# Performance work log

Measured on AMD Instinct MI355X. Metric: run time of the kernel, lower is better.

## Reference

```python
import jax, jax.numpy as jnp
import numpy as np

N_NODES = 100000
N_EDGES = 1600000
IN_FEA = 128
HIDDEN = 128
OUT_FEA = 40


def setup_inputs() -> dict:
    key = jax.random.key(0)
    k1, k2, k3, k4 = jax.random.split(key, 4)
    x = jax.random.normal(k1, (N_NODES, IN_FEA), dtype=jnp.float32)
    edge_index = jax.random.randint(k2, (2, N_EDGES), 0, N_NODES, dtype=jnp.int32)
    # Glorot-ish scaled weights
    W1 = jax.random.normal(k3, (IN_FEA, HIDDEN), dtype=jnp.float32) * (1.0 / np.sqrt(IN_FEA))
    b1 = jnp.zeros((HIDDEN,), dtype=jnp.float32)
    W2 = jax.random.normal(k4, (HIDDEN, OUT_FEA), dtype=jnp.float32) * (1.0 / np.sqrt(HIDDEN))
    b2 = jnp.zeros((OUT_FEA,), dtype=jnp.float32)
    return {"x": x, "edge_index": edge_index, "W1": W1, "b1": b1, "W2": W2, "b2": b2}


def _gcn_conv(x, src, dst, norm, W, b, n_nodes):
    # Linear transform first (PyG GCNConv order), then normalized scatter-add.
    h = x @ W                                   # [N, H]
    msg = h[src] * norm[:, None]                # [E+N, H] gather + scale
    out = jax.ops.segment_sum(msg, dst, num_segments=n_nodes)
    return out + b


def reference(x, edge_index, W1, b1, W2, b2):
    n = x.shape[0]
    loops = jnp.arange(n, dtype=edge_index.dtype)
    src = jnp.concatenate([edge_index[0], loops])  # add self-loops
    dst = jnp.concatenate([edge_index[1], loops])
    # Symmetric degree normalization: deg computed at destination (col)
    deg = jax.ops.segment_sum(jnp.ones_like(dst, dtype=x.dtype), dst, num_segments=n)
    dinv = jax.lax.rsqrt(jnp.maximum(deg, 1.0))
    norm = dinv[src] * dinv[dst]                # [E+N]

    h = jax.nn.relu(_gcn_conv(x, src, dst, norm, W1, b1, n))
    # dropout is identity in eval mode
    logits = _gcn_conv(h, src, dst, norm, W2, b2, n)
    return jax.nn.log_softmax(logits, axis=1)
```

## Files before the change

### kernel.cpp

```cpp
#include <hip/hip_runtime.h>
#include <math.h>

#define N_NODES 100000
#define N_EDGES 1600000
#define CHUNK 4096
#define NCH ((N_EDGES + CHUNK - 1) / CHUNK)
#define DSH 9
#define NBD ((N_NODES + 511) / 512)
#define CAP 9216
#define RCAP 10240

typedef __attribute__((ext_vector_type(8))) short bf16x8;
typedef __attribute__((ext_vector_type(4))) float f32x4;
typedef __attribute__((ext_vector_type(2))) float f32x2;

union U4S8 { uint4 u; bf16x8 s; };

__device__ inline unsigned pk_bf16(float a, float b) {
    unsigned ua = __float_as_uint(a), ub = __float_as_uint(b);
    ua = (ua + 0x7FFFu + ((ua >> 16) & 1u)) >> 16;
    ub = (ub + 0x7FFFu + ((ub >> 16) & 1u)) >> 16;
    return (ua & 0xFFFFu) | (ub << 16);
}
__device__ inline unsigned short bf16_1(float a) {
    unsigned ua = __float_as_uint(a);
    return (unsigned short)((ua + 0x7FFFu + ((ua >> 16) & 1u)) >> 16);
}

__device__ inline void acc8_fp8(f32x2* a, uint2 v) {
    a[0] += __builtin_amdgcn_cvt_pk_f32_fp8((int)v.x, false);
    a[1] += __builtin_amdgcn_cvt_pk_f32_fp8((int)v.x, true);
    a[2] += __builtin_amdgcn_cvt_pk_f32_fp8((int)v.y, false);
    a[3] += __builtin_amdgcn_cvt_pk_f32_fp8((int)v.y, true);
}

__device__ inline void gload_lds16(const void* g, void* l) {
    __builtin_amdgcn_global_load_lds(
        (const __attribute__((address_space(1))) unsigned*)g,
        (__attribute__((address_space(3))) unsigned*)l, 16, 0, 0);
}


__global__ __launch_bounds__(256) void k_prep(const float* __restrict__ W1, const float* __restrict__ W2,
                                              unsigned* __restrict__ W1t, unsigned* __restrict__ W2t,
                                              unsigned* __restrict__ Hb, unsigned* __restrict__ H2b) {
    __shared__ short L[16384];
    int t = threadIdx.x;
    if (blockIdx.x == 0) {
        for (int i = t; i < 16384; i += 256) {
            int k = i >> 7, n = i & 127;
            L[n * 128 + k] = (short)bf16_1(W1[i]);
        }
        __syncthreads();
        uint4* out = (uint4*)W1t;
        const uint4* src = (const uint4*)L;
        for (int i = t; i < 2048; i += 256) out[i] = src[i];
        if (t < 32) Hb[(size_t)N_NODES * 32 + t] = 0u;
    } else {
        for (int i = t; i < 48 * 128; i += 256) L[i] = 0;
        __syncthreads();
        for (int i = t; i < 5120; i += 256) {
            int k = i / 40, n = i - k * 40;
            L[n * 128 + k] = (short)bf16_1(W2[i]);
        }
        __syncthreads();
        uint4* out = (uint4*)W2t;
        const uint4* src = (const uint4*)L;
        for (int i = t; i < 768; i += 256) out[i] = src[i];
        if (t < 10) H2b[(size_t)N_NODES * 10 + t] = 0u;
    }
}


__global__ __launch_bounds__(256) void k_partD(const int* __restrict__ src, const int* __restrict__ dst,
                                               int* __restrict__ gtails, unsigned* __restrict__ staged, int E) {
    __shared__ int hist[NBD];
    __shared__ int tails[NBD];
    int t = threadIdx.x, c = blockIdx.x;
    if (t < NBD) hist[t] = 0;
    __syncthreads();
    int be = c * CHUNK, cw = min(CHUNK, E - be);
    int cw4 = cw >> 2;
    const int4* d4 = (const int4*)(dst + be);
    const int4* s4 = (const int4*)(src + be);
    for (int l = t; l < cw4; l += 256) {
        int4 d = d4[l];
        atomicAdd(&hist[d.x >> DSH], 1);
        atomicAdd(&hist[d.y >> DSH], 1);
        atomicAdd(&hist[d.z >> DSH], 1);
        atomicAdd(&hist[d.w >> DSH], 1);
    }
    __syncthreads();
    if (t < NBD) tails[t] = t * CAP + atomicAdd(&gtails[t], hist[t]);
    __syncthreads();
    for (int l = t; l < cw4; l += 256) {
        int4 d = d4[l];
        int4 s = s4[l];
        int i0 = atomicAdd(&tails[d.x >> DSH], 1);
        staged[i0] = ((unsigned)s.x << DSH) | (unsigned)(d.x & 511);
        int i1 = atomicAdd(&tails[d.y >> DSH], 1);
        staged[i1] = ((unsigned)s.y << DSH) | (unsigned)(d.y & 511);
        int i2 = atomicAdd(&tails[d.z >> DSH], 1);
        staged[i2] = ((unsigned)s.z << DSH) | (unsigned)(d.z & 511);
        int i3 = atomicAdd(&tails[d.w >> DSH], 1);
        staged[i3] = ((unsigned)s.w << DSH) | (unsigned)(d.w & 511);
    }
}

__global__ __launch_bounds__(256) void k_rank(const unsigned* __restrict__ staged, const int* __restrict__ gtails,
                                              int* __restrict__ csr, int* __restrict__ rowptr,
                                              int* __restrict__ cnt, float* __restrict__ dinv, int N) {
    __shared__ unsigned ebuf[RCAP];
    __shared__ int deg[512];
    __shared__ int sc[256];
    __shared__ int tails[512];
    int b = blockIdx.x, t = threadIdx.x;
    int n0 = b << DSH;
    int eb = b * CAP;
    int ne = gtails[b];
    deg[t] = 0; deg[t + 256] = 0;
    __syncthreads();
    bool fit = (ne <= RCAP);
    if (fit) {
        int ne4 = ne >> 2;
        const uint4* st4 = (const uint4*)(staged + eb);
        for (int l = t; l < ne4; l += 256) {
            uint4 pr = st4[l];
            ((uint4*)ebuf)[l] = pr;
            atomicAdd(&deg[pr.x & 511], 1);
            atomicAdd(&deg[pr.y & 511], 1);
            atomicAdd(&deg[pr.z & 511], 1);
            atomicAdd(&deg[pr.w & 511], 1);
        }
        for (int l = (ne4 << 2) + t; l < ne; l += 256) {
            unsigned pr = staged[eb + l];
            ebuf[l] = pr;
            atomicAdd(&deg[pr & 511], 1);
        }
    } else {
        for (int l = t; l < ne; l += 256)
            atomicAdd(&deg[staged[eb + l] & 511], 1);
    }
    __syncthreads();
    int d0 = deg[2 * t], d1 = deg[2 * t + 1];
    int ts = d0 + d1;
    sc[t] = ts; __syncthreads();
    for (int o = 1; o < 256; o <<= 1) {
        int v = (t >= o) ? sc[t - o] : 0;
        __syncthreads();
        sc[t] += v;
        __syncthreads();
    }
    int excl = sc[t] - ts;
    int na = n0 + 2 * t, nb = n0 + 2 * t + 1;
    tails[2 * t] = eb + excl;
    tails[2 * t + 1] = eb + excl + d0;
    if (na < N) { rowptr[na] = eb + excl;      cnt[na] = d0; dinv[na] = rsqrtf((float)(d0 + 1)); }
    if (nb < N) { rowptr[nb] = eb + excl + d0; cnt[nb] = d1; dinv[nb] = rsqrtf((float)(d1 + 1)); }
    __syncthreads();
    if (fit) {
        int ne4 = ne >> 2;
        for (int l = t; l < ne4; l += 256) {
            uint4 pr = ((const uint4*)ebuf)[l];
            int p0 = atomicAdd(&tails[pr.x & 511], 1); csr[p0] = (int)(pr.x >> DSH);
            int p1 = atomicAdd(&tails[pr.y & 511], 1); csr[p1] = (int)(pr.y >> DSH);
            int p2 = atomicAdd(&tails[pr.z & 511], 1); csr[p2] = (int)(pr.z >> DSH);
            int p3 = atomicAdd(&tails[pr.w & 511], 1); csr[p3] = (int)(pr.w >> DSH);
        }
        for (int l = (ne4 << 2) + t; l < ne; l += 256) {
            unsigned pr = ebuf[l];
            int pos = atomicAdd(&tails[pr & 511], 1);
            csr[pos] = (int)(pr >> DSH);
        }
    } else {
        for (int l = t; l < ne; l += 256) {
            unsigned pr = staged[eb + l];
            int pos = atomicAdd(&tails[pr & 511], 1);
            csr[pos] = (int)(pr >> DSH);
        }
    }
}


__global__ __launch_bounds__(256) void k_gemm1(const float* __restrict__ x, const unsigned* __restrict__ W1t,
                                               const float* __restrict__ dinv, unsigned* __restrict__ Hb, int M) {
    __shared__ uint4 As[2048];
    __shared__ uint4 Bs[2048];
    int t = threadIdx.x;
    int w = t >> 6, lane = t & 63;
    int m = lane & 15, kg = lane >> 4;
    int blk0 = blockIdx.x * 64;

    #pragma unroll
    for (int it = 0; it < 8; ++it) {
        int G = it * 256 + t;
        int row = G >> 5, slot = G & 31;
        int rowg = min(blk0 + row, M - 1);
        const float* srcp = x + (size_t)rowg * 128 + ((slot ^ (row & 7)) << 2);
        gload_lds16(srcp, (char*)As + (size_t)G * 16);
    }
    #pragma unroll
    for (int it = 0; it < 8; ++it) {
        int G = it * 256 + t;
        int rb = G >> 4, slot = G & 15;
        const unsigned* srcp = W1t + rb * 64 + ((slot ^ (rb & 7)) << 2);
        gload_lds16(srcp, (char*)Bs + (size_t)G * 16);
    }
    __syncthreads();

    int ra = (w << 4) + m;
    int rs = m & 7;
    f32x4 acc[8];
    #pragma unroll
    for (int j = 0; j < 8; j++) acc[j] = (f32x4){0.f, 0.f, 0.f, 0.f};

    #pragma unroll
    for (int ks = 0; ks < 4; ks++) {
        uint4 qa = As[ra * 32 + ((ks * 8 + kg * 2) ^ rs)];
        uint4 qb = As[ra * 32 + ((ks * 8 + kg * 2 + 1) ^ rs)];
        float4 f0 = *(float4*)&qa;
        float4 f1 = *(float4*)&qb;
        U4S8 a0; a0.u = make_uint4(pk_bf16(f0.x, f0.y), pk_bf16(f0.z, f0.w),
                                   pk_bf16(f1.x, f1.y), pk_bf16(f1.z, f1.w));
        #pragma unroll
        for (int nt = 0; nt < 8; nt++) {
            U4S8 b; b.u = Bs[(nt * 16 + m) * 16 + ((ks * 4 + kg) ^ rs)];
            acc[nt] = __builtin_amdgcn_mfma_f32_16x16x32_bf16(a0.s, b.s, acc[nt], 0, 0, 0);
        }
    }
    int m_base = blk0 + (w << 4);
    #pragma unroll
    for (int r = 0; r < 4; r++) {
        int row = m_base + kg * 4 + r;
        float di = dinv[min(row, M - 1)];
        bool on = (row < M) && ((m & 3) == 0);
        #pragma unroll
        for (int nt = 0; nt < 8; nt++) {
            float v = acc[nt][r] * di;
            float v1 = __shfl_xor(v, 1);
            unsigned wlo = (unsigned)__builtin_amdgcn_cvt_pk_fp8_f32(v, v1, 0, false);
            unsigned whi = __shfl_xor(wlo, 2);
            unsigned u = (wlo & 0xFFFFu) | (whi << 16);
            if (on) Hb[(size_t)row * 32 + nt * 4 + (m >> 2)] = u;
        }
    }
}


__global__ __launch_bounds__(256) void k_prop1(const unsigned* __restrict__ Hb, const int* __restrict__ rowptr,
                                               const int* __restrict__ cnt, const int* __restrict__ csr,
                                               const float* __restrict__ dinv, const float* __restrict__ b1,
                                               unsigned* __restrict__ h1b, int N) {
    int lane = threadIdx.x & 63;
    int g = lane >> 4, q = lane & 15;
    int i = blockIdx.x * 16 + (threadIdx.x >> 6) * 4 + g;
    if (i >= N) return;
    const uint2* H2 = (const uint2*)Hb;

    f32x2 a0[4], a1[4], a2[4], a3[4];
    #pragma unroll
    for (int k = 0; k < 4; k++) {
        a0[k] = (f32x2){0.f, 0.f}; a1[k] = (f32x2){0.f, 0.f};
        a2[k] = (f32x2){0.f, 0.f}; a3[k] = (f32x2){0.f, 0.f};
    }

    {
        uint2 sv = H2[(size_t)i * 16 + q];
        acc8_fp8(a0, sv);
    }

    int s = rowptr[i];
    int e = s + cnt[i];
    int p = s;
    for (; p + 8 <= e; p += 8) {
        int j0 = csr[p];     int j1 = csr[p + 1];
        int j2 = csr[p + 2]; int j3 = csr[p + 3];
        int j4 = csr[p + 4]; int j5 = csr[p + 5];
        int j6 = csr[p + 6]; int j7 = csr[p + 7];
        uint2 v0 = H2[(size_t)j0 * 16 + q];
        uint2 v1 = H2[(size_t)j1 * 16 + q];
        uint2 v2 = H2[(size_t)j2 * 16 + q];
        uint2 v3 = H2[(size_t)j3 * 16 + q];
        uint2 v4 = H2[(size_t)j4 * 16 + q];
        uint2 v5 = H2[(size_t)j5 * 16 + q];
        uint2 v6 = H2[(size_t)j6 * 16 + q];
        uint2 v7 = H2[(size_t)j7 * 16 + q];
        acc8_fp8(a0, v0); acc8_fp8(a1, v1); acc8_fp8(a2, v2); acc8_fp8(a3, v3);
        acc8_fp8(a0, v4); acc8_fp8(a1, v5); acc8_fp8(a2, v6); acc8_fp8(a3, v7);
    }
    if (p + 4 <= e) {
        int j0 = csr[p];     int j1 = csr[p + 1];
        int j2 = csr[p + 2]; int j3 = csr[p + 3];
        uint2 v0 = H2[(size_t)j0 * 16 + q];
        uint2 v1 = H2[(size_t)j1 * 16 + q];
        uint2 v2 = H2[(size_t)j2 * 16 + q];
        uint2 v3 = H2[(size_t)j3 * 16 + q];
        acc8_fp8(a0, v0); acc8_fp8(a1, v1); acc8_fp8(a2, v2); acc8_fp8(a3, v3);
        p += 4;
    }
    for (; p < e; ++p) {
        int j = csr[p];
        uint2 v = H2[(size_t)j * 16 + q];
        acc8_fp8(a0, v);
    }
    #pragma unroll
    for (int k = 0; k < 4; k++) a0[k] = (a0[k] + a1[k]) + (a2[k] + a3[k]);

    float di = dinv[i];
    float4 bA = ((const float4*)b1)[q * 2];
    float4 bB = ((const float4*)b1)[q * 2 + 1];
    float o0 = fmaxf(di * a0[0].x + bA.x, 0.f);
    float o1 = fmaxf(di * a0[0].y + bA.y, 0.f);
    float o2 = fmaxf(di * a0[1].x + bA.z, 0.f);
    float o3 = fmaxf(di * a0[1].y + bA.w, 0.f);
    float o4 = fmaxf(di * a0[2].x + bB.x, 0.f);
    float o5 = fmaxf(di * a0[2].y + bB.y, 0.f);
    float o6 = fmaxf(di * a0[3].x + bB.z, 0.f);
    float o7 = fmaxf(di * a0[3].y + bB.w, 0.f);
    ((uint4*)h1b)[(size_t)i * 16 + q] =
        make_uint4(pk_bf16(o0, o1), pk_bf16(o2, o3), pk_bf16(o4, o5), pk_bf16(o6, o7));
}


__global__ __launch_bounds__(256) void k_gemm2(const unsigned* __restrict__ h1b, const unsigned* __restrict__ W2t,
                                               const float* __restrict__ dinv, unsigned* __restrict__ H2b, int M) {
    __shared__ uint4 As[1024];
    __shared__ uint4 Bs[768];
    int t = threadIdx.x;
    int w = t >> 6, lane = t & 63;
    int m = lane & 15, kg = lane >> 4;
    int blk0 = blockIdx.x * 64;

    #pragma unroll
    for (int it = 0; it < 4; ++it) {
        int G = it * 256 + t;
        int row = G >> 4, slot = G & 15;
        int rowg = min(blk0 + row, M - 1);
        const unsigned* srcp = h1b + (size_t)rowg * 64 + ((slot ^ (row & 7)) << 2);
        gload_lds16(srcp, (char*)As + (size_t)G * 16);
    }
    #pragma unroll
    for (int it = 0; it < 3; ++it) {
        int G = it * 256 + t;
        int rb = G >> 4, slot = G & 15;
        const unsigned* srcp = W2t + rb * 64 + ((slot ^ (rb & 7)) << 2);
        gload_lds16(srcp, (char*)Bs + (size_t)G * 16);
    }
    __syncthreads();

    int ra = (w << 4) + m;
    int rs = m & 7;
    f32x4 acc[3];
    #pragma unroll
    for (int j = 0; j < 3; j++) acc[j] = (f32x4){0.f, 0.f, 0.f, 0.f};

    #pragma unroll
    for (int ks = 0; ks < 4; ks++) {
        U4S8 a0; a0.u = As[ra * 16 + ((ks * 4 + kg) ^ rs)];
        #pragma unroll
        for (int nt = 0; nt < 3; nt++) {
            U4S8 b; b.u = Bs[(nt * 16 + m) * 16 + ((ks * 4 + kg) ^ rs)];
            acc[nt] = __builtin_amdgcn_mfma_f32_16x16x32_bf16(a0.s, b.s, acc[nt], 0, 0, 0);
        }
    }
    int m_base = blk0 + (w << 4);
    #pragma unroll
    for (int r = 0; r < 4; r++) {
        int row = m_base + kg * 4 + r;
        float di = dinv[min(row, M - 1)];
        #pragma unroll
        for (int nt = 0; nt < 3; nt++) {
            float v = acc[nt][r] * di;
            float v1 = __shfl_xor(v, 1);
            unsigned wlo = (unsigned)__builtin_amdgcn_cvt_pk_fp8_f32(v, v1, 0, false);
            unsigned whi = __shfl_xor(wlo, 2);
            unsigned u = (wlo & 0xFFFFu) | (whi << 16);
            unsigned u2 = __shfl_xor(u, 4);
            bool on = (row < M) && ((m & 7) == 0) && (nt < 2 || m == 0);
            if (on) ((uint2*)H2b)[(size_t)row * 5 + nt * 2 + (m >> 3)] = make_uint2(u, u2);
        }
    }
}


__global__ __launch_bounds__(256) void k_prop2(const unsigned* __restrict__ H2b, const int* __restrict__ rowptr,
                                               const int* __restrict__ cnt, const int* __restrict__ csr,
                                               const float* __restrict__ dinv, const float* __restrict__ b2,
                                               float* __restrict__ out, int N) {
    int lane = threadIdx.x & 63;
    int wv = threadIdx.x >> 6;
    int grp = lane / 5;
    int q = lane - grp * 5;
    if (grp >= 12) return;
    int i = blockIdx.x * 48 + wv * 12 + grp;
    if (i >= N) return;
    const uint2* H2 = (const uint2*)H2b;

    f32x2 a0[4], a1[4], a2[4], a3[4];
    #pragma unroll
    for (int k = 0; k < 4; k++) {
        a0[k] = (f32x2){0.f, 0.f}; a1[k] = (f32x2){0.f, 0.f};
        a2[k] = (f32x2){0.f, 0.f}; a3[k] = (f32x2){0.f, 0.f};
    }

    acc8_fp8(a0, H2[(size_t)i * 5 + q]);

    int s = rowptr[i];
    int e = s + cnt[i];
    int p = s;
    for (; p + 8 <= e; p += 8) {
        int j0 = csr[p];     int j1 = csr[p + 1];
        int j2 = csr[p + 2]; int j3 = csr[p + 3];
        int j4 = csr[p + 4]; int j5 = csr[p + 5];
        int j6 = csr[p + 6]; int j7 = csr[p + 7];
        uint2 v0 = H2[(size_t)j0 * 5 + q];
        uint2 v1 = H2[(size_t)j1 * 5 + q];
        uint2 v2 = H2[(size_t)j2 * 5 + q];
        uint2 v3 = H2[(size_t)j3 * 5 + q];
        uint2 v4 = H2[(size_t)j4 * 5 + q];
        uint2 v5 = H2[(size_t)j5 * 5 + q];
        uint2 v6 = H2[(size_t)j6 * 5 + q];
        uint2 v7 = H2[(size_t)j7 * 5 + q];
        acc8_fp8(a0, v0); acc8_fp8(a1, v1); acc8_fp8(a2, v2); acc8_fp8(a3, v3);
        acc8_fp8(a0, v4); acc8_fp8(a1, v5); acc8_fp8(a2, v6); acc8_fp8(a3, v7);
    }
    if (p + 4 <= e) {
        int j0 = csr[p];     int j1 = csr[p + 1];
        int j2 = csr[p + 2]; int j3 = csr[p + 3];
        uint2 v0 = H2[(size_t)j0 * 5 + q];
        uint2 v1 = H2[(size_t)j1 * 5 + q];
        uint2 v2 = H2[(size_t)j2 * 5 + q];
        uint2 v3 = H2[(size_t)j3 * 5 + q];
        acc8_fp8(a0, v0); acc8_fp8(a1, v1); acc8_fp8(a2, v2); acc8_fp8(a3, v3);
        p += 4;
    }
    for (; p < e; ++p) {
        uint2 v = H2[(size_t)csr[p] * 5 + q];
        acc8_fp8(a0, v);
    }
    #pragma unroll
    for (int k = 0; k < 4; k++) a0[k] = (a0[k] + a1[k]) + (a2[k] + a3[k]);

    float di = dinv[i];
    float4 b0 = ((const float4*)b2)[q * 2];
    float4 b1v = ((const float4*)b2)[q * 2 + 1];
    float l[8];
    l[0] = di * a0[0].x + b0.x;  l[1] = di * a0[0].y + b0.y;
    l[2] = di * a0[1].x + b0.z;  l[3] = di * a0[1].y + b0.w;
    l[4] = di * a0[2].x + b1v.x; l[5] = di * a0[2].y + b1v.y;
    l[6] = di * a0[3].x + b1v.z; l[7] = di * a0[3].y + b1v.w;

    float mx = l[0];
    #pragma unroll
    for (int k = 1; k < 8; k++) mx = fmaxf(mx, l[k]);
    int gb = grp * 5;
    mx = fmaxf(mx, __shfl(mx, gb + (q + 1) % 5));
    mx = fmaxf(mx, __shfl(mx, gb + (q + 2) % 5));
    mx = fmaxf(mx, __shfl(mx, gb + (q + 4) % 5));

    float sm = 0.f;
    #pragma unroll
    for (int k = 0; k < 8; k++) sm += expf(l[k] - mx);
    float st = sm;
    st += __shfl(sm, gb + (q + 1) % 5);
    st += __shfl(sm, gb + (q + 2) % 5);
    st += __shfl(sm, gb + (q + 3) % 5);
    st += __shfl(sm, gb + (q + 4) % 5);
    float lse = mx + logf(st);

    ((float4*)out)[(size_t)i * 10 + q * 2]     = make_float4(l[0] - lse, l[1] - lse, l[2] - lse, l[3] - lse);
    ((float4*)out)[(size_t)i * 10 + q * 2 + 1] = make_float4(l[4] - lse, l[5] - lse, l[6] - lse, l[7] - lse);
}


extern "C" void kernel_launch(void* const* d_in, const int* in_sizes, int n_in,
                              void* d_out, int out_size, void* d_ws, size_t ws_size,
                              hipStream_t stream) {
    const float* x  = (const float*)d_in[0];
    const int*   ei = (const int*)d_in[1];
    const float* W1 = (const float*)d_in[2];
    const float* b1 = (const float*)d_in[3];
    const float* W2 = (const float*)d_in[4];
    const float* b2 = (const float*)d_in[5];
    float* out = (float*)d_out;
    char* ws = (char*)d_ws;
    const int N = N_NODES, E = N_EDGES;

    size_t o = 0;
    auto alloc = [&](size_t bytes) { size_t cur = o; o += (bytes + 511) & ~(size_t)511; return cur; };
    int*       cnt    = (int*)(ws + alloc((size_t)N * 4));
    int*       rowptr = (int*)(ws + alloc((size_t)N * 4));
    float*     dinv   = (float*)(ws + alloc((size_t)N * 4));
    int*       gtails = (int*)(ws + alloc((size_t)NBD * 4));
    unsigned*  staged = (unsigned*)(ws + alloc((size_t)NBD * CAP * 4));
    int*       csr    = (int*)(ws + alloc((size_t)NBD * CAP * 4));
    unsigned*  W1t    = (unsigned*)(ws + alloc(128 * 128 * 2));
    unsigned*  W2t    = (unsigned*)(ws + alloc(48 * 128 * 2));
    unsigned*  Hb     = (unsigned*)(ws + alloc((size_t)(N + 1) * 32 * 4));
    unsigned*  h1b    = (unsigned*)(ws + alloc((size_t)N * 64 * 4));
    unsigned*  H2b    = (unsigned*)(ws + alloc((size_t)(N + 1) * 10 * 4));

    const int* src = ei;
    const int* dst = ei + E;

    hipMemsetAsync(gtails, 0, (size_t)NBD * 4, stream);
    k_prep <<<2, 256, 0, stream>>>(W1, W2, W1t, W2t, Hb, H2b);
    k_partD<<<NCH, 256, 0, stream>>>(src, dst, gtails, staged, E);
    k_rank <<<NBD, 256, 0, stream>>>(staged, gtails, csr, rowptr, cnt, dinv, N);

    k_gemm1<<<(N + 63) / 64, 256, 0, stream>>>(x, W1t, dinv, Hb, N);
    k_prop1<<<(N + 15) / 16, 256, 0, stream>>>(Hb, rowptr, cnt, csr, dinv, b1, h1b, N);
    k_gemm2<<<(N + 63) / 64, 256, 0, stream>>>(h1b, W2t, dinv, H2b, N);
    k_prop2<<<(N + 47) / 48, 256, 0, stream>>>(H2b, rowptr, cnt, csr, dinv, b2, out, N);

    (void)in_sizes; (void)n_in; (void)out_size; (void)ws_size;
}
```

Baseline: 229.9 us.

## Make GEMM kernels persistent with double-buffered LDS prefetch; fold memset into prep

Both GEMM kernels now run as persistent grids (256 and 512 blocks) that loop over 64-row tiles. The next tile's A block is prefetched into a second LDS buffer with async global-to-LDS loads while the current tile is computed, and the B weights are loaded once per block instead of once per tile. The separate hipMemsetAsync that zeroes the partition tails is replaced by a store inside k_prep, removing one launch. The trade-offs are larger LDS use per block, which can lower occupancy, and a fixed grid size that may not fill every CU evenly.

```diff
diff --git a/kernel.cpp b/kernel.cpp
--- a/kernel.cpp
+++ b/kernel.cpp
@@ -43,10 +43,12 @@
 
 __global__ __launch_bounds__(256) void k_prep(const float* __restrict__ W1, const float* __restrict__ W2,
                                               unsigned* __restrict__ W1t, unsigned* __restrict__ W2t,
-                                              unsigned* __restrict__ Hb, unsigned* __restrict__ H2b) {
+                                              unsigned* __restrict__ Hb, unsigned* __restrict__ H2b,
+                                              int* __restrict__ gtails) {
     __shared__ short L[16384];
     int t = threadIdx.x;
     if (blockIdx.x == 0) {
+        if (t < NBD) gtails[t] = 0;
         for (int i = t; i < 16384; i += 256) {
             int k = i >> 7, n = i & 127;
             L[n * 128 + k] = (short)bf16_1(W1[i]);
@@ -184,65 +186,85 @@
 
 __global__ __launch_bounds__(256) void k_gemm1(const float* __restrict__ x, const unsigned* __restrict__ W1t,
                                                const float* __restrict__ dinv, unsigned* __restrict__ Hb, int M) {
-    __shared__ uint4 As[2048];
     __shared__ uint4 Bs[2048];
+    __shared__ uint4 As[2][2048];
     int t = threadIdx.x;
     int w = t >> 6, lane = t & 63;
     int m = lane & 15, kg = lane >> 4;
-    int blk0 = blockIdx.x * 64;
-
-    #pragma unroll
-    for (int it = 0; it < 8; ++it) {
-        int G = it * 256 + t;
-        int row = G >> 5, slot = G & 31;
-        int rowg = min(blk0 + row, M - 1);
-        const float* srcp = x + (size_t)rowg * 128 + ((slot ^ (row & 7)) << 2);
-        gload_lds16(srcp, (char*)As + (size_t)G * 16);
-    }
+    const int NT = (M + 63) >> 6;
+    const int GRID = (int)gridDim.x;
+
     #pragma unroll
     for (int it = 0; it < 8; ++it) {
         int G = it * 256 + t;
         int rb = G >> 4, slot = G & 15;
-        const unsigned* srcp = W1t + rb * 64 + ((slot ^ (rb & 7)) << 2);
-        gload_lds16(srcp, (char*)Bs + (size_t)G * 16);
+        gload_lds16(W1t + rb * 64 + ((slot ^ (rb & 7)) << 2), (char*)Bs + (size_t)G * 16);
+    }
+    int tix = blockIdx.x;
+    if (tix < NT) {
+        #pragma unroll
+        for (int it = 0; it < 8; ++it) {
+            int G = it * 256 + t;
+            int row = G >> 5, slot = G & 31;
+            int rowg = min(tix * 64 + row, M - 1);
+            gload_lds16(x + (size_t)rowg * 128 + ((slot ^ (row & 7)) << 2), (char*)As[0] + (size_t)G * 16);
+        }
     }
     __syncthreads();
 
     int ra = (w << 4) + m;
     int rs = m & 7;
-    f32x4 acc[8];
-    #pragma unroll
-    for (int j = 0; j < 8; j++) acc[j] = (f32x4){0.f, 0.f, 0.f, 0.f};
-
-    #pragma unroll
-    for (int ks = 0; ks < 4; ks++) {
-        uint4 qa = As[ra * 32 + ((ks * 8 + kg * 2) ^ rs)];
-        uint4 qb = As[ra * 32 + ((ks * 8 + kg * 2 + 1) ^ rs)];
-        float4 f0 = *(float4*)&qa;
-        float4 f1 = *(float4*)&qb;
-        U4S8 a0; a0.u = make_uint4(pk_bf16(f0.x, f0.y), pk_bf16(f0.z, f0.w),
-                                   pk_bf16(f1.x, f1.y), pk_bf16(f1.z, f1.w));
-        #pragma unroll
-        for (int nt = 0; nt < 8; nt++) {
-            U4S8 b; b.u = Bs[(nt * 16 + m) * 16 + ((ks * 4 + kg) ^ rs)];
-            acc[nt] = __builtin_amdgcn_mfma_f32_16x16x32_bf16(a0.s, b.s, acc[nt], 0, 0, 0);
-        }
-    }
-    int m_base = blk0 + (w << 4);
-    #pragma unroll
-    for (int r = 0; r < 4; r++) {
-        int row = m_base + kg * 4 + r;
-        float di = dinv[min(row, M - 1)];
-        bool on = (row < M) && ((m & 3) == 0);
-        #pragma unroll
-        for (int nt = 0; nt < 8; nt++) {
-            float v = acc[nt][r] * di;
-            float v1 = __shfl_xor(v, 1);
-            unsigned wlo = (unsigned)__builtin_amdgcn_cvt_pk_fp8_f32(v, v1, 0, false);
-            unsigned whi = __shfl_xor(wlo, 2);
-            unsigned u = (wlo & 0xFFFFu) | (whi << 16);
-            if (on) Hb[(size_t)row * 32 + nt * 4 + (m >> 2)] = u;
-        }
+    int cur = 0;
+    for (; tix < NT; tix += GRID) {
+        int tn = tix + GRID;
+        if (tn < NT) {
+            #pragma unroll
+            for (int it = 0; it < 8; ++it) {
+                int G = it * 256 + t;
+                int row = G >> 5, slot = G & 31;
+                int rowg = min(tn * 64 + row, M - 1);
+                gload_lds16(x + (size_t)rowg * 128 + ((slot ^ (row & 7)) << 2),
+                            (char*)As[cur ^ 1] + (size_t)G * 16);
+            }
+        }
+
+        f32x4 acc[8];
+        #pragma unroll
+        for (int j = 0; j < 8; j++) acc[j] = (f32x4){0.f, 0.f, 0.f, 0.f};
+
+        const uint4* Ac = As[cur];
+        #pragma unroll
+        for (int ks = 0; ks < 4; ks++) {
+            uint4 qa = Ac[ra * 32 + ((ks * 8 + kg * 2) ^ rs)];
+            uint4 qb = Ac[ra * 32 + ((ks * 8 + kg * 2 + 1) ^ rs)];
+            float4 f0 = *(float4*)&qa;
+            float4 f1 = *(float4*)&qb;
+            U4S8 a0; a0.u = make_uint4(pk_bf16(f0.x, f0.y), pk_bf16(f0.z, f0.w),
+                                       pk_bf16(f1.x, f1.y), pk_bf16(f1.z, f1.w));
+            #pragma unroll
+            for (int nt = 0; nt < 8; nt++) {
+                U4S8 b; b.u = Bs[(nt * 16 + m) * 16 + ((ks * 4 + kg) ^ rs)];
+                acc[nt] = __builtin_amdgcn_mfma_f32_16x16x32_bf16(a0.s, b.s, acc[nt], 0, 0, 0);
+            }
+        }
+        int m_base = tix * 64 + (w << 4);
+        #pragma unroll
+        for (int r = 0; r < 4; r++) {
+            int row = m_base + kg * 4 + r;
+            float di = dinv[min(row, M - 1)];
+            bool on = (row < M) && ((m & 3) == 0);
+            #pragma unroll
+            for (int nt = 0; nt < 8; nt++) {
+                float v = acc[nt][r] * di;
+                float v1 = __shfl_xor(v, 1);
+                unsigned wlo = (unsigned)__builtin_amdgcn_cvt_pk_fp8_f32(v, v1, 0, false);
+                unsigned whi = __shfl_xor(wlo, 2);
+                unsigned u = (wlo & 0xFFFFu) | (whi << 16);
+                if (on) Hb[(size_t)row * 32 + nt * 4 + (m >> 2)] = u;
+            }
+        }
+        __syncthreads();
+        cur ^= 1;
     }
 }
 
@@ -324,61 +346,81 @@
 
 __global__ __launch_bounds__(256) void k_gemm2(const unsigned* __restrict__ h1b, const unsigned* __restrict__ W2t,
                                                const float* __restrict__ dinv, unsigned* __restrict__ H2b, int M) {
-    __shared__ uint4 As[1024];
     __shared__ uint4 Bs[768];
+    __shared__ uint4 As[2][1024];
     int t = threadIdx.x;
     int w = t >> 6, lane = t & 63;
     int m = lane & 15, kg = lane >> 4;
-    int blk0 = blockIdx.x * 64;
-
-    #pragma unroll
-    for (int it = 0; it < 4; ++it) {
-        int G = it * 256 + t;
-        int row = G >> 4, slot = G & 15;
-        int rowg = min(blk0 + row, M - 1);
-        const unsigned* srcp = h1b + (size_t)rowg * 64 + ((slot ^ (row & 7)) << 2);
-        gload_lds16(srcp, (char*)As + (size_t)G * 16);
-    }
+    const int NT = (M + 63) >> 6;
+    const int GRID = (int)gridDim.x;
+
     #pragma unroll
     for (int it = 0; it < 3; ++it) {
         int G = it * 256 + t;
         int rb = G >> 4, slot = G & 15;
-        const unsigned* srcp = W2t + rb * 64 + ((slot ^ (rb & 7)) << 2);
-        gload_lds16(srcp, (char*)Bs + (size_t)G * 16);
+        gload_lds16(W2t + rb * 64 + ((slot ^ (rb & 7)) << 2), (char*)Bs + (size_t)G * 16);
+    }
+    int tix = blockIdx.x;
+    if (tix < NT) {
+        #pragma unroll
+        for (int it = 0; it < 4; ++it) {
+            int G = it * 256 + t;
+            int row = G >> 4, slot = G & 15;
+            int rowg = min(tix * 64 + row, M - 1);
+            gload_lds16(h1b + (size_t)rowg * 64 + ((slot ^ (row & 7)) << 2), (char*)As[0] + (size_t)G * 16);
+        }
     }
     __syncthreads();
 
     int ra = (w << 4) + m;
     int rs = m & 7;
-    f32x4 acc[3];
-    #pragma unroll
-    for (int j = 0; j < 3; j++) acc[j] = (f32x4){0.f, 0.f, 0.f, 0.f};
-
-    #pragma unroll
-    for (int ks = 0; ks < 4; ks++) {
-        U4S8 a0; a0.u = As[ra * 16 + ((ks * 4 + kg) ^ rs)];
-        #pragma unroll
-        for (int nt = 0; nt < 3; nt++) {
-            U4S8 b; b.u = Bs[(nt * 16 + m) * 16 + ((ks * 4 + kg) ^ rs)];
-            acc[nt] = __builtin_amdgcn_mfma_f32_16x16x32_bf16(a0.s, b.s, acc[nt], 0, 0, 0);
-        }
-    }
-    int m_base = blk0 + (w << 4);
-    #pragma unroll
-    for (int r = 0; r < 4; r++) {
-        int row = m_base + kg * 4 + r;
-        float di = dinv[min(row, M - 1)];
-        #pragma unroll
-        for (int nt = 0; nt < 3; nt++) {
-            float v = acc[nt][r] * di;
-            float v1 = __shfl_xor(v, 1);
-            unsigned wlo = (unsigned)__builtin_amdgcn_cvt_pk_fp8_f32(v, v1, 0, false);
-            unsigned whi = __shfl_xor(wlo, 2);
-            unsigned u = (wlo & 0xFFFFu) | (whi << 16);
-            unsigned u2 = __shfl_xor(u, 4);
-            bool on = (row < M) && ((m & 7) == 0) && (nt < 2 || m == 0);
-            if (on) ((uint2*)H2b)[(size_t)row * 5 + nt * 2 + (m >> 3)] = make_uint2(u, u2);
-        }
+    int cur = 0;
+    for (; tix < NT; tix += GRID) {
+        int tn = tix + GRID;
+        if (tn < NT) {
+            #pragma unroll
+            for (int it = 0; it < 4; ++it) {
+                int G = it * 256 + t;
+                int row = G >> 4, slot = G & 15;
+                int rowg = min(tn * 64 + row, M - 1);
+                gload_lds16(h1b + (size_t)rowg * 64 + ((slot ^ (row & 7)) << 2),
+                            (char*)As[cur ^ 1] + (size_t)G * 16);
+            }
+        }
+
+        f32x4 acc[3];
+        #pragma unroll
+        for (int j = 0; j < 3; j++) acc[j] = (f32x4){0.f, 0.f, 0.f, 0.f};
+
+        const uint4* Ac = As[cur];
+        #pragma unroll
+        for (int ks = 0; ks < 4; ks++) {
+            U4S8 a0; a0.u = Ac[ra * 16 + ((ks * 4 + kg) ^ rs)];
+            #pragma unroll
+            for (int nt = 0; nt < 3; nt++) {
+                U4S8 b; b.u = Bs[(nt * 16 + m) * 16 + ((ks * 4 + kg) ^ rs)];
+                acc[nt] = __builtin_amdgcn_mfma_f32_16x16x32_bf16(a0.s, b.s, acc[nt], 0, 0, 0);
+            }
+        }
+        int m_base = tix * 64 + (w << 4);
+        #pragma unroll
+        for (int r = 0; r < 4; r++) {
+            int row = m_base + kg * 4 + r;
+            float di = dinv[min(row, M - 1)];
+            #pragma unroll
+            for (int nt = 0; nt < 3; nt++) {
+                float v = acc[nt][r] * di;
+                float v1 = __shfl_xor(v, 1);
+                unsigned wlo = (unsigned)__builtin_amdgcn_cvt_pk_fp8_f32(v, v1, 0, false);
+                unsigned whi = __shfl_xor(wlo, 2);
+                unsigned u = (wlo & 0xFFFFu) | (whi << 16);
+                unsigned u2 = __shfl_xor(u, 4);
+                bool on = (row < M) && ((m & 7) == 0) && (nt < 2 || m == 0);
+                if (on) ((uint2*)H2b)[(size_t)row * 5 + nt * 2 + (m >> 3)] = make_uint2(u, u2);
+            }
+        }
+        __syncthreads();
+        cur ^= 1;
     }
 }
 
@@ -503,14 +545,13 @@
     const int* src = ei;
     const int* dst = ei + E;
 
-    hipMemsetAsync(gtails, 0, (size_t)NBD * 4, stream);
-    k_prep <<<2, 256, 0, stream>>>(W1, W2, W1t, W2t, Hb, H2b);
+    k_prep <<<2, 256, 0, stream>>>(W1, W2, W1t, W2t, Hb, H2b, gtails);
     k_partD<<<NCH, 256, 0, stream>>>(src, dst, gtails, staged, E);
     k_rank <<<NBD, 256, 0, stream>>>(staged, gtails, csr, rowptr, cnt, dinv, N);
 
-    k_gemm1<<<(N + 63) / 64, 256, 0, stream>>>(x, W1t, dinv, Hb, N);
+    k_gemm1<<<256, 256, 0, stream>>>(x, W1t, dinv, Hb, N);
     k_prop1<<<(N + 15) / 16, 256, 0, stream>>>(Hb, rowptr, cnt, csr, dinv, b1, h1b, N);
-    k_gemm2<<<(N + 63) / 64, 256, 0, stream>>>(h1b, W2t, dinv, H2b, N);
+    k_gemm2<<<512, 256, 0, stream>>>(h1b, W2t, dinv, H2b, N);
     k_prop2<<<(N + 47) / 48, 256, 0, stream>>>(H2b, rowptr, cnt, csr, dinv, b2, out, N);
 
     (void)in_sizes; (void)n_in; (void)out_size; (void)ws_size;
```

Measured after the change: 242.4 us. +5.4%, slower.
